# Performance work log

Measured on AMD Instinct MI355X. Metric: run time of the kernel, lower is better.

The kernel has to match this reference:

```python
import jax, jax.numpy as jnp
import numpy as np

B, S, D, H, L, FF = 4, 2048, 256, 8, 4, 512
DK = D // H
EPS = 1e-5


def _ln(x, scale, bias):
    m = jnp.mean(x, axis=-1, keepdims=True)
    v = jnp.mean(jnp.square(x - m), axis=-1, keepdims=True)
    return (x - m) / jnp.sqrt(v + EPS) * scale + bias


def setup_inputs() -> dict:
    key = jax.random.key(0)
    ks = jax.random.split(key, 12)
    w = lambda k, shape: jax.random.normal(k, shape, dtype=jnp.float32) * 0.02
    return {
        "x": jax.random.normal(ks[0], (B, S, D), dtype=jnp.float32),
        "ln0_s": jnp.ones((D,), jnp.float32), "ln0_b": jnp.zeros((D,), jnp.float32),
        "ln1_s": jnp.ones((L, D), jnp.float32), "ln1_b": jnp.zeros((L, D), jnp.float32),
        "ln2_s": jnp.ones((L, D), jnp.float32), "ln2_b": jnp.zeros((L, D), jnp.float32),
        "wq": w(ks[1], (L, D, D)), "bq": jnp.zeros((L, D), jnp.float32),
        "wk": w(ks[2], (L, D, D)), "bk": jnp.zeros((L, D), jnp.float32),
        "wv": w(ks[3], (L, D, D)), "bv": jnp.zeros((L, D), jnp.float32),
        "wo": w(ks[4], (L, D, D)), "bo": jnp.zeros((L, D), jnp.float32),
        "w1": w(ks[5], (L, D, FF)), "b1": jnp.zeros((L, FF), jnp.float32),
        "w2": w(ks[6], (L, FF, D)), "b2": jnp.zeros((L, D), jnp.float32),
    }


def reference(x, ln0_s, ln0_b, ln1_s, ln1_b, ln2_s, ln2_b,
              wq, bq, wk, bk, wv, bv, wo, bo, w1, b1, w2, b2):
    scale = 1.0 / np.sqrt(DK).astype(np.float32)
    x = _ln(x, ln0_s, ln0_b)  # Encoder's leading LayerNorm

    def step(h, p):
        (l1s, l1b, l2s, l2b, Wq, Bq, Wk, Bk, Wv, Bv, Wo, Bo, W1, B1, W2, B2) = p
        # --- pre-norm multi-head attention ---
        x2 = _ln(h, l1s, l1b)
        q = (x2 @ Wq + Bq).reshape(B, S, H, DK)
        k = (x2 @ Wk + Bk).reshape(B, S, H, DK)
        v = (x2 @ Wv + Bv).reshape(B, S, H, DK)
        scores = jnp.einsum('bqhd,bkhd->bhqk', q, k) * scale  # [B,H,S,S]
        attn = jax.nn.softmax(scores, axis=-1)
        o = jnp.einsum('bhqk,bkhd->bqhd', attn, v).reshape(B, S, D)
        h = h + (o @ Wo + Bo)
        # --- pre-norm feed-forward (hidden fixed at 512, ReLU) ---
        x2 = _ln(h, l2s, l2b)
        h = h + (jax.nn.relu(x2 @ W1 + B1) @ W2 + B2)
        return h, None

    layer_params = (ln1_s, ln1_b, ln2_s, ln2_b, wq, bq, wk, bk,
                    wv, bv, wo, bo, w1, b1, w2, b2)
    x, _ = jax.lax.scan(step, x, layer_params)
    return x
```

## Files before the change

kernel.cpp:

```cpp
#include <hip/hip_runtime.h>
#include <hip/hip_bf16.h>
#include <math.h>

#define SEQ 2048
#define DIM 256
#define NH 8
#define DK 32
#define FF 512

typedef __bf16 bf16_t;
typedef bf16_t bf16x8 __attribute__((ext_vector_type(8)));
typedef bf16_t bf16x4 __attribute__((ext_vector_type(4)));
typedef float f32x4 __attribute__((ext_vector_type(4)));

#define QK_SCALE_LOG2 0.25503226632462494f
#if __has_builtin(__builtin_amdgcn_exp2f)
#define FAST_EXP2(x) __builtin_amdgcn_exp2f(x)
#else
#define FAST_EXP2(x) __expf((x) * 0.6931471805599453f)
#endif

template <int OUT_BF>
__global__ __launch_bounds__(256) void ln_kernel(
    const float* __restrict__ x, const float* __restrict__ s,
    const float* __restrict__ b, float* __restrict__ outf,
    bf16_t* __restrict__ outb) {
  int wave = threadIdx.x >> 6;
  int lane = threadIdx.x & 63;
  int row = blockIdx.x * 4 + wave;
  const float* xr = x + (size_t)row * DIM + lane * 4;
  float4 xv = *(const float4*)xr;
  float sum = xv.x + xv.y + xv.z + xv.w;
  float sq = xv.x * xv.x + xv.y * xv.y + xv.z * xv.z + xv.w * xv.w;
#pragma unroll
  for (int off = 1; off < 64; off <<= 1) {
    sum += __shfl_xor(sum, off);
    sq += __shfl_xor(sq, off);
  }
  float mean = sum * (1.0f / 256.0f);
  float var = sq * (1.0f / 256.0f) - mean * mean;
  float inv = rsqrtf(var + 1e-5f);
  float4 sv = *(const float4*)(s + lane * 4);
  float4 bv = *(const float4*)(b + lane * 4);
  float4 o;
  o.x = (xv.x - mean) * inv * sv.x + bv.x;
  o.y = (xv.y - mean) * inv * sv.y + bv.y;
  o.z = (xv.z - mean) * inv * sv.z + bv.z;
  o.w = (xv.w - mean) * inv * sv.w + bv.w;
  if (OUT_BF) {
    bf16x4 ob = {(bf16_t)o.x, (bf16_t)o.y, (bf16_t)o.z, (bf16_t)o.w};
    *(bf16x4*)(outb + (size_t)row * DIM + lane * 4) = ob;
  } else {
    *(float4*)(outf + (size_t)row * DIM + lane * 4) = o;
  }
}

__global__ __launch_bounds__(256) void wtrans_all_kernel(
    const float* __restrict__ wq, const float* __restrict__ wk,
    const float* __restrict__ wv, const float* __restrict__ wo,
    const float* __restrict__ w1, const float* __restrict__ w2,
    bf16_t* __restrict__ WqT, bf16_t* __restrict__ WkT,
    bf16_t* __restrict__ WvT, bf16_t* __restrict__ WoT,
    bf16_t* __restrict__ W1T, bf16_t* __restrict__ W2T) {
  __shared__ float tile[64][65];
  int idx = blockIdx.x;
  int layer = idx >> 7;
  int r = idx & 127;
  const float* src;
  bf16_t* dst;
  int N, k0, n0;
  if (r < 64) {
    int which = r >> 4, t = r & 15;
    N = 256;
    k0 = (t & 3) * 64;
    n0 = (t >> 2) * 64;
    src = (which == 0 ? wq : which == 1 ? wk : which == 2 ? wv : wo) + (size_t)layer * 65536;
    dst = (which == 0 ? WqT : which == 1 ? WkT : which == 2 ? WvT : WoT) + (size_t)layer * 65536;
  } else if (r < 96) {
    int t = r - 64;
    N = 512;
    k0 = (t & 3) * 64;
    n0 = (t >> 2) * 64;
    src = w1 + (size_t)layer * 131072;
    dst = W1T + (size_t)layer * 131072;
  } else {
    int t = r - 96;
    N = 256;
    k0 = (t & 7) * 64;
    n0 = (t >> 3) * 64;
    src = w2 + (size_t)layer * 131072;
    dst = W2T + (size_t)layer * 131072;
  }
  int K = (r >= 96) ? 512 : 256;

  int tr = threadIdx.x >> 4;
  int tc4 = (threadIdx.x & 15) * 4;
#pragma unroll
  for (int i = 0; i < 4; i++) {
    int kl = i * 16 + tr;
    float4 v = *(const float4*)(src + (size_t)(k0 + kl) * N + n0 + tc4);
    tile[kl][tc4 + 0] = v.x; tile[kl][tc4 + 1] = v.y;
    tile[kl][tc4 + 2] = v.z; tile[kl][tc4 + 3] = v.w;
  }
  __syncthreads();
#pragma unroll
  for (int i = 0; i < 4; i++) {
    int nl = i * 16 + tr;
    bf16x4 o = {(bf16_t)tile[tc4 + 0][nl], (bf16_t)tile[tc4 + 1][nl],
                (bf16_t)tile[tc4 + 2][nl], (bf16_t)tile[tc4 + 3][nl]};
    *(bf16x4*)(dst + (size_t)(n0 + nl) * K + k0 + tc4) = o;
  }
}

__device__ __forceinline__ void stage4(const bf16_t* __restrict__ src,
                                       bf16_t* dst, int tid, int ldk, int kofs) {
#pragma unroll
  for (int st = 0; st < 4; st++) {
#pragma unroll
    for (int u = 0; u < 2; u++) {
      int i = u * 256 + tid;
      int m = i >> 3, cd = i & 7, cs = cd ^ (m & 7);
      const bf16_t* g = src + (size_t)m * ldk + kofs + st * 64 + cs * 8;
      __builtin_amdgcn_global_load_lds(
          (const __attribute__((address_space(1))) unsigned int*)g,
          (__attribute__((address_space(3))) unsigned int*)(dst + st * 4096 + i * 8),
          16, 0, 0);
    }
  }
}

__device__ __forceinline__ void compute4(const bf16_t* As, const bf16_t* Bs,
                                         int mw, int nw, int n16, int quad,
                                         f32x4 (&acc)[2][2]) {
  const int sw = n16 & 7;
#pragma unroll
  for (int st = 0; st < 4; st++) {
#pragma unroll
    for (int ks = 0; ks < 2; ks++) {
      int cd = (ks * 4 + quad) ^ sw;
      bf16x8 a0 = *(const bf16x8*)(As + st * 4096 + (mw + n16) * 64 + cd * 8);
      bf16x8 a1 = *(const bf16x8*)(As + st * 4096 + (mw + 16 + n16) * 64 + cd * 8);
      bf16x8 b0 = *(const bf16x8*)(Bs + st * 4096 + (nw + n16) * 64 + cd * 8);
      bf16x8 b1 = *(const bf16x8*)(Bs + st * 4096 + (nw + 16 + n16) * 64 + cd * 8);
      acc[0][0] = __builtin_amdgcn_mfma_f32_16x16x32_bf16(a0, b0, acc[0][0], 0, 0, 0);
      acc[0][1] = __builtin_amdgcn_mfma_f32_16x16x32_bf16(a0, b1, acc[0][1], 0, 0, 0);
      acc[1][0] = __builtin_amdgcn_mfma_f32_16x16x32_bf16(a1, b0, acc[1][0], 0, 0, 0);
      acc[1][1] = __builtin_amdgcn_mfma_f32_16x16x32_bf16(a1, b1, acc[1][1], 0, 0, 0);
    }
  }
}

template <int MODE, int N, int K>
__global__ __launch_bounds__(256) void gemm8_kernel(
    const bf16_t* __restrict__ A, const bf16_t* __restrict__ BT,
    const float* __restrict__ bias, const float* __restrict__ resid,
    float* __restrict__ outf, bf16_t* __restrict__ outb) {
  __shared__ __align__(16) bf16_t As[16384];
  __shared__ __align__(16) bf16_t Bs[16384];
  int tid = threadIdx.x;
  int lane = tid & 63;
  int n16 = lane & 15, quad = lane >> 4;
  int w = tid >> 6;
  int m0 = blockIdx.y * 64, n0 = blockIdx.x * 64;
  int mw = (w >> 1) * 32, nw = (w & 1) * 32;
  f32x4 acc[2][2] = {};

  const bf16_t* Arow = A + (size_t)m0 * K;
  const bf16_t* Brow = BT + (size_t)n0 * K;

  stage4(Arow, As, tid, K, 0);
  stage4(Brow, Bs, tid, K, 0);
  __syncthreads();
  compute4(As, Bs, mw, nw, n16, quad, acc);
  if (K == 512) {
    __syncthreads();
    stage4(Arow, As, tid, K, 256);
    stage4(Brow, Bs, tid, K, 256);
    __syncthreads();
    compute4(As, Bs, mw, nw, n16, quad, acc);
  }

  int m_base = m0 + mw;
  int n_base = n0 + nw;
  float bias_v[2];
#pragma unroll
  for (int nt = 0; nt < 2; nt++) bias_v[nt] = bias[n_base + nt * 16 + n16];
#pragma unroll
  for (int mt = 0; mt < 2; mt++)
#pragma unroll
    for (int nt = 0; nt < 2; nt++) {
      int n = n_base + nt * 16 + n16;
#pragma unroll
      for (int r = 0; r < 4; r++) {
        int m = m_base + mt * 16 + quad * 4 + r;
        float val = acc[mt][nt][r] + bias_v[nt];
        if (MODE == 0) {
          size_t idx = (size_t)m * N + n;
          outf[idx] = resid[idx] + val;
        } else {
          outb[(size_t)m * N + n] = (bf16_t)fmaxf(val, 0.0f);
        }
      }
    }
}

__global__ __launch_bounds__(256) void qkv8_kernel(
    const bf16_t* __restrict__ A,
    const bf16_t* __restrict__ WqT, const bf16_t* __restrict__ WkT,
    const bf16_t* __restrict__ WvT,
    const float* __restrict__ bq, const float* __restrict__ bk,
    const float* __restrict__ bv,
    bf16_t* __restrict__ qo, bf16_t* __restrict__ ko,
    bf16_t* __restrict__ vo) {
  __shared__ __align__(16) bf16_t As[16384];
  __shared__ __align__(16) bf16_t Bs[16384];
  int which = blockIdx.x >> 2;
  int nblk = blockIdx.x & 3;
  const bf16_t* BT = (which == 0) ? WqT : (which == 1) ? WkT : WvT;
  const float* bias = (which == 0) ? bq : (which == 1) ? bk : bv;

  int tid = threadIdx.x;
  int lane = tid & 63;
  int n16 = lane & 15, quad = lane >> 4;
  int w = tid >> 6;
  int m0 = blockIdx.y * 64, n0 = nblk * 64;
  int mw = (w >> 1) * 32, nw = (w & 1) * 32;
  f32x4 acc[2][2] = {};

  stage4(A + (size_t)m0 * 256, As, tid, 256, 0);
  stage4(BT + (size_t)n0 * 256, Bs, tid, 256, 0);
  __syncthreads();
  compute4(As, Bs, mw, nw, n16, quad, acc);

  int m_base = m0 + mw;
  int n_base = n0 + nw;
  float bias_v[2];
#pragma unroll
  for (int nt = 0; nt < 2; nt++) bias_v[nt] = bias[n_base + nt * 16 + n16];

#pragma unroll
  for (int mt = 0; mt < 2; mt++)
#pragma unroll
    for (int nt = 0; nt < 2; nt++) {
      int n = n_base + nt * 16 + n16;
      int hh = n >> 5, dk = n & 31;
      if (which == 2) {
        int s0 = m_base + mt * 16 + quad * 4;
        int bb = s0 >> 11, ss0 = s0 & 2047;
        bf16x4 o;
#pragma unroll
        for (int r = 0; r < 4; r++) o[r] = (bf16_t)(acc[mt][nt][r] + bias_v[nt]);
        *(bf16x4*)(vo + ((size_t)(bb * NH + hh) * DK + dk) * SEQ + ss0) = o;
      } else {
        bf16_t* dst = (which == 0) ? qo : ko;
        float sc = (which == 0) ? QK_SCALE_LOG2 : 1.0f;
#pragma unroll
        for (int r = 0; r < 4; r++) {
          int m = m_base + mt * 16 + quad * 4 + r;
          int bb = m >> 11, ss = m & 2047;
          dst[((size_t)(bb * NH + hh) * SEQ + ss) * DK + dk] =
              (bf16_t)((acc[mt][nt][r] + bias_v[nt]) * sc);
        }
      }
    }
}

__global__ __launch_bounds__(128) void flash7_kernel(
    const bf16_t* __restrict__ Q, const bf16_t* __restrict__ K,
    const bf16_t* __restrict__ VT, bf16_t* __restrict__ OB) {
  __shared__ __align__(16) bf16_t Plds[2][2][32][72];
  int bh = blockIdx.x;
  int q0 = blockIdx.y * 64;
  int w = threadIdx.x >> 6;
  int lane = threadIdx.x & 63;
  int n16 = lane & 15;
  int quad = lane >> 4;

  const bf16_t* Qb = Q + (size_t)bh * SEQ * DK;
  const bf16_t* Kb = K + (size_t)bh * SEQ * DK;
  const bf16_t* Vb = VT + (size_t)bh * DK * SEQ;
  int qr0 = q0 + w * 32;

  bf16x8 qfrag[2];
#pragma unroll
  for (int qg = 0; qg < 2; qg++)
    qfrag[qg] = *(const bf16x8*)(Qb + (size_t)(qr0 + qg * 16 + n16) * DK + quad * 8);

  bf16_t one = (bf16_t)1.0f;
  bf16x8 ones = {one, one, one, one, one, one, one, one};

  f32x4 oacc[2][2] = {};
  f32x4 lacc[2] = {};

  bf16x8 kfc[4], vfc[2][2];
#pragma unroll
  for (int t = 0; t < 4; t++)
    kfc[t] = *(const bf16x8*)(Kb + (size_t)(t * 16 + n16) * DK + quad * 8);
#pragma unroll
  for (int c = 0; c < 2; c++) {
    vfc[c][0] = *(const bf16x8*)(Vb + (size_t)n16 * SEQ + c * 32 + quad * 8);
    vfc[c][1] = *(const bf16x8*)(Vb + (size_t)(16 + n16) * SEQ + c * 32 + quad * 8);
  }

#pragma unroll 2
  for (int kb0 = 0; kb0 < SEQ; kb0 += 64) {
    int buf = (kb0 >> 6) & 1;
    int nb = kb0 + 64;
    bool has_next = nb < SEQ;
    bf16x8 kfn[4], vfn[2][2];
    if (has_next) {
#pragma unroll
      for (int t = 0; t < 4; t++)
        kfn[t] = *(const bf16x8*)(Kb + (size_t)(nb + t * 16 + n16) * DK + quad * 8);
#pragma unroll
      for (int c = 0; c < 2; c++) {
        vfn[c][0] = *(const bf16x8*)(Vb + (size_t)n16 * SEQ + nb + c * 32 + quad * 8);
        vfn[c][1] = *(const bf16x8*)(Vb + (size_t)(16 + n16) * SEQ + nb + c * 32 + quad * 8);
      }
    }
#pragma unroll
    for (int qg = 0; qg < 2; qg++) {
#pragma unroll
      for (int t = 0; t < 4; t++) {
        f32x4 sc = __builtin_amdgcn_mfma_f32_16x16x32_bf16(
            kfc[t], qfrag[qg], (f32x4){0.f, 0.f, 0.f, 0.f}, 0, 0, 0);
        bf16x4 pf;
#pragma unroll
        for (int r = 0; r < 4; r++) pf[r] = (bf16_t)FAST_EXP2(sc[r]);
        *(bf16x4*)&Plds[buf][w][qg * 16 + n16][t * 16 + quad * 4] = pf;
      }
    }
#pragma unroll
    for (int qg = 0; qg < 2; qg++)
#pragma unroll
      for (int c = 0; c < 2; c++) {
        bf16x8 pf8 = *(const bf16x8*)&Plds[buf][w][qg * 16 + n16][c * 32 + quad * 8];
        lacc[qg] = __builtin_amdgcn_mfma_f32_16x16x32_bf16(pf8, ones, lacc[qg], 0, 0, 0);
        oacc[qg][0] = __builtin_amdgcn_mfma_f32_16x16x32_bf16(pf8, vfc[c][0], oacc[qg][0], 0, 0, 0);
        oacc[qg][1] = __builtin_amdgcn_mfma_f32_16x16x32_bf16(pf8, vfc[c][1], oacc[qg][1], 0, 0, 0);
      }
    if (has_next) {
#pragma unroll
      for (int t = 0; t < 4; t++) kfc[t] = kfn[t];
#pragma unroll
      for (int c = 0; c < 2; c++) {
        vfc[c][0] = vfn[c][0];
        vfc[c][1] = vfn[c][1];
      }
    }
  }

  int bb = bh >> 3, hh = bh & 7;
#pragma unroll
  for (int qg = 0; qg < 2; qg++)
#pragma unroll
    for (int r = 0; r < 4; r++) {
      float linv = 1.0f / lacc[qg][r];
      int row = qr0 + qg * 16 + quad * 4 + r;
      bf16_t* op = OB + ((size_t)(bb * SEQ + row)) * DIM + hh * DK;
      op[n16] = (bf16_t)(oacc[qg][0][r] * linv);
      op[16 + n16] = (bf16_t)(oacc[qg][1][r] * linv);
    }
}

extern "C" void kernel_launch(void* const* d_in, const int* in_sizes, int n_in,
                              void* d_out, int out_size, void* d_ws, size_t ws_size,
                              hipStream_t stream) {
  const float* x     = (const float*)d_in[0];
  const float* ln0_s = (const float*)d_in[1];
  const float* ln0_b = (const float*)d_in[2];
  const float* ln1_s = (const float*)d_in[3];
  const float* ln1_b = (const float*)d_in[4];
  const float* ln2_s = (const float*)d_in[5];
  const float* ln2_b = (const float*)d_in[6];
  const float* wq = (const float*)d_in[7];
  const float* bq = (const float*)d_in[8];
  const float* wk = (const float*)d_in[9];
  const float* bk = (const float*)d_in[10];
  const float* wv = (const float*)d_in[11];
  const float* bv = (const float*)d_in[12];
  const float* wo = (const float*)d_in[13];
  const float* bo = (const float*)d_in[14];
  const float* w1 = (const float*)d_in[15];
  const float* b1 = (const float*)d_in[16];
  const float* w2 = (const float*)d_in[17];
  const float* b2 = (const float*)d_in[18];

  float* out = (float*)d_out;
  const size_t ACT = (size_t)8192 * DIM;

  bf16_t* wsb = (bf16_t*)d_ws;
  bf16_t* x2b = wsb;
  bf16_t* obf = x2b + ACT;
  bf16_t* qbf = obf + ACT;
  bf16_t* kbf = qbf + ACT;
  bf16_t* vbf = kbf + ACT;
  bf16_t* h1b = vbf + ACT;
  bf16_t* WqT = h1b + 2 * ACT;
  bf16_t* WkT = WqT + 4 * 65536;
  bf16_t* WvT = WkT + 4 * 65536;
  bf16_t* WoT = WvT + 4 * 65536;
  bf16_t* W1T = WoT + 4 * 65536;
  bf16_t* W2T = W1T + 4 * 131072;

  dim3 blk(256);
  dim3 blkF(128);
  dim3 gLN(2048);
  dim3 gG256(4, 128);
  dim3 gG512(8, 128);
  dim3 gQKV(12, 128);
  dim3 gAtt(32, 32);

  wtrans_all_kernel<<<dim3(512), blk, 0, stream>>>(wq, wk, wv, wo, w1, w2,
                                                   WqT, WkT, WvT, WoT, W1T, W2T);

  ln_kernel<0><<<gLN, blk, 0, stream>>>(x, ln0_s, ln0_b, out, nullptr);

  for (int l = 0; l < 4; l++) {
    bf16_t* WqTl = WqT + (size_t)l * 65536;
    bf16_t* WkTl = WkT + (size_t)l * 65536;
    bf16_t* WvTl = WvT + (size_t)l * 65536;
    bf16_t* WoTl = WoT + (size_t)l * 65536;
    bf16_t* W1Tl = W1T + (size_t)l * 131072;
    bf16_t* W2Tl = W2T + (size_t)l * 131072;

    ln_kernel<1><<<gLN, blk, 0, stream>>>(out, ln1_s + l * DIM, ln1_b + l * DIM, nullptr, x2b);
    qkv8_kernel<<<gQKV, blk, 0, stream>>>(x2b, WqTl, WkTl, WvTl,
                                          bq + l * DIM, bk + l * DIM, bv + l * DIM,
                                          qbf, kbf, vbf);
    flash7_kernel<<<gAtt, blkF, 0, stream>>>(qbf, kbf, vbf, obf);
    gemm8_kernel<0, 256, 256><<<gG256, blk, 0, stream>>>(obf, WoTl, bo + l * DIM, out, out, nullptr);
    ln_kernel<1><<<gLN, blk, 0, stream>>>(out, ln2_s + l * DIM, ln2_b + l * DIM, nullptr, x2b);
    gemm8_kernel<1, 512, 256><<<gG512, blk, 0, stream>>>(x2b, W1Tl, b1 + l * FF, nullptr, nullptr, h1b);
    gemm8_kernel<0, 256, 512><<<gG256, blk, 0, stream>>>(h1b, W2Tl, b2 + l * DIM, out, out, nullptr);
  }
}
```

Baseline: 468.2 us.

## Enlarge GEMM tiles to 128x128 with double-buffered K-step pipeline

Replaces the 64x64 GEMM tiles with 128x128 tiles, where each wave computes a 64x64 sub-tile via a 4x4 MFMA accumulator grid. The K loop now runs in steps of 64 and double-buffers the LDS stages, so the next global-to-LDS load overlaps the current compute. The aim is more operand reuse per LDS read and fewer global loads. The cost is a quarter as many blocks, which may under-fill the CUs for these small GEMMs, plus higher register pressure.

Result: no change. 468.6 us (+0.1%).

```diff
diff --git a/kernel.cpp b/kernel.cpp
--- a/kernel.cpp
+++ b/kernel.cpp
@@ -112,88 +112,101 @@
   }
 }
 
-__device__ __forceinline__ void stage4(const bf16_t* __restrict__ src,
-                                       bf16_t* dst, int tid, int ldk, int kofs) {
-#pragma unroll
-  for (int st = 0; st < 4; st++) {
-#pragma unroll
-    for (int u = 0; u < 2; u++) {
-      int i = u * 256 + tid;
-      int m = i >> 3, cd = i & 7, cs = cd ^ (m & 7);
-      const bf16_t* g = src + (size_t)m * ldk + kofs + st * 64 + cs * 8;
-      __builtin_amdgcn_global_load_lds(
-          (const __attribute__((address_space(1))) unsigned int*)g,
-          (__attribute__((address_space(3))) unsigned int*)(dst + st * 4096 + i * 8),
-          16, 0, 0);
-    }
-  }
-}
-
-__device__ __forceinline__ void compute4(const bf16_t* As, const bf16_t* Bs,
-                                         int mw, int nw, int n16, int quad,
-                                         f32x4 (&acc)[2][2]) {
-  const int sw = n16 & 7;
-#pragma unroll
-  for (int st = 0; st < 4; st++) {
-#pragma unroll
-    for (int ks = 0; ks < 2; ks++) {
-      int cd = (ks * 4 + quad) ^ sw;
-      bf16x8 a0 = *(const bf16x8*)(As + st * 4096 + (mw + n16) * 64 + cd * 8);
-      bf16x8 a1 = *(const bf16x8*)(As + st * 4096 + (mw + 16 + n16) * 64 + cd * 8);
-      bf16x8 b0 = *(const bf16x8*)(Bs + st * 4096 + (nw + n16) * 64 + cd * 8);
-      bf16x8 b1 = *(const bf16x8*)(Bs + st * 4096 + (nw + 16 + n16) * 64 + cd * 8);
-      acc[0][0] = __builtin_amdgcn_mfma_f32_16x16x32_bf16(a0, b0, acc[0][0], 0, 0, 0);
-      acc[0][1] = __builtin_amdgcn_mfma_f32_16x16x32_bf16(a0, b1, acc[0][1], 0, 0, 0);
-      acc[1][0] = __builtin_amdgcn_mfma_f32_16x16x32_bf16(a1, b0, acc[1][0], 0, 0, 0);
-      acc[1][1] = __builtin_amdgcn_mfma_f32_16x16x32_bf16(a1, b1, acc[1][1], 0, 0, 0);
-    }
+__device__ __forceinline__ void stage128(const bf16_t* __restrict__ src,
+                                         bf16_t* dst, int tid, int ldk, int k0) {
+#pragma unroll
+  for (int u = 0; u < 4; u++) {
+    int i = u * 256 + tid;
+    int m = i >> 3, cd = i & 7, cs = cd ^ (m & 7);
+    const bf16_t* g = src + (size_t)m * ldk + k0 + cs * 8;
+    __builtin_amdgcn_global_load_lds(
+        (const __attribute__((address_space(1))) unsigned int*)g,
+        (__attribute__((address_space(3))) unsigned int*)(dst + i * 8),
+        16, 0, 0);
+  }
+}
+
+__device__ __forceinline__ void compute128(const bf16_t* As, const bf16_t* Bs,
+                                           int wr, int wc, int n16, int quad,
+                                           f32x4 (&acc)[4][4]) {
+#pragma unroll
+  for (int ks = 0; ks < 2; ks++) {
+    bf16x8 af[4], bf[4];
+#pragma unroll
+    for (int mt = 0; mt < 4; mt++) {
+      int row = wr * 64 + mt * 16 + n16;
+      int cd = (ks * 4 + quad) ^ (row & 7);
+      af[mt] = *(const bf16x8*)(As + row * 64 + cd * 8);
+    }
+#pragma unroll
+    for (int nt = 0; nt < 4; nt++) {
+      int row = wc * 64 + nt * 16 + n16;
+      int cd = (ks * 4 + quad) ^ (row & 7);
+      bf[nt] = *(const bf16x8*)(Bs + row * 64 + cd * 8);
+    }
+#pragma unroll
+    for (int mt = 0; mt < 4; mt++)
+#pragma unroll
+      for (int nt = 0; nt < 4; nt++)
+        acc[mt][nt] = __builtin_amdgcn_mfma_f32_16x16x32_bf16(
+            af[mt], bf[nt], acc[mt][nt], 0, 0, 0);
+  }
+}
+
+template <int K>
+__device__ __forceinline__ void gemm9_body(
+    const bf16_t* __restrict__ A, const bf16_t* __restrict__ BT,
+    int m0, int n0, int tid, bf16_t* As, bf16_t* Bs, f32x4 (&acc)[4][4]) {
+  int lane = tid & 63;
+  int n16 = lane & 15, quad = lane >> 4;
+  int w = tid >> 6;
+  int wr = w >> 1, wc = w & 1;
+  const bf16_t* Arow = A + (size_t)m0 * K;
+  const bf16_t* Brow = BT + (size_t)n0 * K;
+
+  stage128(Arow, As, tid, K, 0);
+  stage128(Brow, Bs, tid, K, 0);
+
+  const int steps = K / 64;
+#pragma unroll
+  for (int s = 0; s < steps; s++) {
+    int buf = s & 1;
+    if (s + 1 < steps) {
+      stage128(Arow, As + (buf ^ 1) * 8192, tid, K, (s + 1) * 64);
+      stage128(Brow, Bs + (buf ^ 1) * 8192, tid, K, (s + 1) * 64);
+    }
+    __syncthreads();
+    compute128(As + buf * 8192, Bs + buf * 8192, wr, wc, n16, quad, acc);
+    if (s + 2 < steps) __syncthreads();
   }
 }
 
 template <int MODE, int N, int K>
-__global__ __launch_bounds__(256) void gemm8_kernel(
+__global__ __launch_bounds__(256) void gemm9_kernel(
     const bf16_t* __restrict__ A, const bf16_t* __restrict__ BT,
     const float* __restrict__ bias, const float* __restrict__ resid,
     float* __restrict__ outf, bf16_t* __restrict__ outb) {
-  __shared__ __align__(16) bf16_t As[16384];
-  __shared__ __align__(16) bf16_t Bs[16384];
+  __shared__ __align__(16) bf16_t As[2 * 8192];
+  __shared__ __align__(16) bf16_t Bs[2 * 8192];
   int tid = threadIdx.x;
   int lane = tid & 63;
   int n16 = lane & 15, quad = lane >> 4;
   int w = tid >> 6;
-  int m0 = blockIdx.y * 64, n0 = blockIdx.x * 64;
-  int mw = (w >> 1) * 32, nw = (w & 1) * 32;
-  f32x4 acc[2][2] = {};
-
-  const bf16_t* Arow = A + (size_t)m0 * K;
-  const bf16_t* Brow = BT + (size_t)n0 * K;
-
-  stage4(Arow, As, tid, K, 0);
-  stage4(Brow, Bs, tid, K, 0);
-  __syncthreads();
-  compute4(As, Bs, mw, nw, n16, quad, acc);
-  if (K == 512) {
-    __syncthreads();
-    stage4(Arow, As, tid, K, 256);
-    stage4(Brow, Bs, tid, K, 256);
-    __syncthreads();
-    compute4(As, Bs, mw, nw, n16, quad, acc);
-  }
-
-  int m_base = m0 + mw;
-  int n_base = n0 + nw;
-  float bias_v[2];
-#pragma unroll
-  for (int nt = 0; nt < 2; nt++) bias_v[nt] = bias[n_base + nt * 16 + n16];
-#pragma unroll
-  for (int mt = 0; mt < 2; mt++)
-#pragma unroll
-    for (int nt = 0; nt < 2; nt++) {
-      int n = n_base + nt * 16 + n16;
+  int wr = w >> 1, wc = w & 1;
+  int m0 = blockIdx.y * 128, n0 = blockIdx.x * 128;
+  f32x4 acc[4][4] = {};
+  gemm9_body<K>(A, BT, m0, n0, tid, As, Bs, acc);
+
+#pragma unroll
+  for (int nt = 0; nt < 4; nt++) {
+    int n = n0 + wc * 64 + nt * 16 + n16;
+    float bv = bias[n];
+#pragma unroll
+    for (int mt = 0; mt < 4; mt++) {
 #pragma unroll
       for (int r = 0; r < 4; r++) {
-        int m = m_base + mt * 16 + quad * 4 + r;
-        float val = acc[mt][nt][r] + bias_v[nt];
+        int m = m0 + wr * 64 + mt * 16 + quad * 4 + r;
+        float val = acc[mt][nt][r] + bv;
         if (MODE == 0) {
           size_t idx = (size_t)m * N + n;
           outf[idx] = resid[idx] + val;
@@ -202,9 +215,10 @@
         }
       }
     }
-}
-
-__global__ __launch_bounds__(256) void qkv8_kernel(
+  }
+}
+
+__global__ __launch_bounds__(256) void qkv9_kernel(
     const bf16_t* __restrict__ A,
     const bf16_t* __restrict__ WqT, const bf16_t* __restrict__ WkT,
     const bf16_t* __restrict__ WvT,
@@ -212,10 +226,10 @@
     const float* __restrict__ bv,
     bf16_t* __restrict__ qo, bf16_t* __restrict__ ko,
     bf16_t* __restrict__ vo) {
-  __shared__ __align__(16) bf16_t As[16384];
-  __shared__ __align__(16) bf16_t Bs[16384];
-  int which = blockIdx.x >> 2;
-  int nblk = blockIdx.x & 3;
+  __shared__ __align__(16) bf16_t As[2 * 8192];
+  __shared__ __align__(16) bf16_t Bs[2 * 8192];
+  int which = blockIdx.x >> 1;
+  int nblk = blockIdx.x & 1;
   const bf16_t* BT = (which == 0) ? WqT : (which == 1) ? WkT : WvT;
   const float* bias = (which == 0) ? bq : (which == 1) ? bk : bv;
 
@@ -223,46 +237,38 @@
   int lane = tid & 63;
   int n16 = lane & 15, quad = lane >> 4;
   int w = tid >> 6;
-  int m0 = blockIdx.y * 64, n0 = nblk * 64;
-  int mw = (w >> 1) * 32, nw = (w & 1) * 32;
-  f32x4 acc[2][2] = {};
-
-  stage4(A + (size_t)m0 * 256, As, tid, 256, 0);
-  stage4(BT + (size_t)n0 * 256, Bs, tid, 256, 0);
-  __syncthreads();
-  compute4(As, Bs, mw, nw, n16, quad, acc);
-
-  int m_base = m0 + mw;
-  int n_base = n0 + nw;
-  float bias_v[2];
-#pragma unroll
-  for (int nt = 0; nt < 2; nt++) bias_v[nt] = bias[n_base + nt * 16 + n16];
-
-#pragma unroll
-  for (int mt = 0; mt < 2; mt++)
-#pragma unroll
-    for (int nt = 0; nt < 2; nt++) {
-      int n = n_base + nt * 16 + n16;
-      int hh = n >> 5, dk = n & 31;
+  int wr = w >> 1, wc = w & 1;
+  int m0 = blockIdx.y * 128, n0 = nblk * 128;
+  f32x4 acc[4][4] = {};
+  gemm9_body<256>(A, BT, m0, n0, tid, As, Bs, acc);
+
+#pragma unroll
+  for (int nt = 0; nt < 4; nt++) {
+    int n = n0 + wc * 64 + nt * 16 + n16;
+    float bv_ = bias[n];
+    int hh = n >> 5, dk = n & 31;
+#pragma unroll
+    for (int mt = 0; mt < 4; mt++) {
       if (which == 2) {
-        int s0 = m_base + mt * 16 + quad * 4;
+        int s0 = m0 + wr * 64 + mt * 16 + quad * 4;
         int bb = s0 >> 11, ss0 = s0 & 2047;
         bf16x4 o;
 #pragma unroll
-        for (int r = 0; r < 4; r++) o[r] = (bf16_t)(acc[mt][nt][r] + bias_v[nt]);
+        for (int r = 0; r < 4; r++) o[r] = (bf16_t)(acc[mt][nt][r] + bv_);
         *(bf16x4*)(vo + ((size_t)(bb * NH + hh) * DK + dk) * SEQ + ss0) = o;
       } else {
         bf16_t* dst = (which == 0) ? qo : ko;
         float sc = (which == 0) ? QK_SCALE_LOG2 : 1.0f;
 #pragma unroll
         for (int r = 0; r < 4; r++) {
-          int m = m_base + mt * 16 + quad * 4 + r;
+          int m = m0 + wr * 64 + mt * 16 + quad * 4 + r;
           int bb = m >> 11, ss = m & 2047;
           dst[((size_t)(bb * NH + hh) * SEQ + ss) * DK + dk] =
-              (bf16_t)((acc[mt][nt][r] + bias_v[nt]) * sc);
+              (bf16_t)((acc[mt][nt][r] + bv_) * sc);
         }
       }
     }
+  }
 }
 
 __global__ __launch_bounds__(128) void flash7_kernel(
@@ -406,9 +412,9 @@
   dim3 blk(256);
   dim3 blkF(128);
   dim3 gLN(2048);
-  dim3 gG256(4, 128);
-  dim3 gG512(8, 128);
-  dim3 gQKV(12, 128);
+  dim3 gG256(2, 64);
+  dim3 gG512(4, 64);
+  dim3 gQKV(6, 64);
   dim3 gAtt(32, 32);
 
   wtrans_all_kernel<<<dim3(512), blk, 0, stream>>>(wq, wk, wv, wo, w1, w2,
@@ -425,13 +431,13 @@
     bf16_t* W2Tl = W2T + (size_t)l * 131072;
 
     ln_kernel<1><<<gLN, blk, 0, stream>>>(out, ln1_s + l * DIM, ln1_b + l * DIM, nullptr, x2b);
-    qkv8_kernel<<<gQKV, blk, 0, stream>>>(x2b, WqTl, WkTl, WvTl,
+    qkv9_kernel<<<gQKV, blk, 0, stream>>>(x2b, WqTl, WkTl, WvTl,
                                           bq + l * DIM, bk + l * DIM, bv + l * DIM,
                                           qbf, kbf, vbf);
     flash7_kernel<<<gAtt, blkF, 0, stream>>>(qbf, kbf, vbf, obf);
-    gemm8_kernel<0, 256, 256><<<gG256, blk, 0, stream>>>(obf, WoTl, bo + l * DIM, out, out, nullptr);
+    gemm9_kernel<0, 256, 256><<<gG256, blk, 0, stream>>>(obf, WoTl, bo + l * DIM, out, out, nullptr);
     ln_kernel<1><<<gLN, blk, 0, stream>>>(out, ln2_s + l * DIM, ln2_b + l * DIM, nullptr, x2b);
-    gemm8_kernel<1, 512, 256><<<gG512, blk, 0, stream>>>(x2b, W1Tl, b1 + l * FF, nullptr, nullptr, h1b);
-    gemm8_kernel<0, 256, 512><<<gG256, blk, 0, stream>>>(h1b, W2Tl, b2 + l * DIM, out, out, nullptr);
-  }
-}
+    gemm9_kernel<1, 512, 256><<<gG512, blk, 0, stream>>>(x2b, W1Tl, b1 + l * FF, nullptr, nullptr, h1b);
+    gemm9_kernel<0, 256, 512><<<gG256, blk, 0, stream>>>(h1b, W2Tl, b2 + l * DIM, out, out, nullptr);
+  }
+}
```
